# Kernel optimization log

Hardware: AMD Instinct MI355X
Metric: run time of the kernel (lower is better)

Reference implementation:

```python
import jax, jax.numpy as jnp
import numpy as np
from jax import lax

# ---- static config (mirrors init_kwargs) ----
B, C, IMG, P = 8, 3, 512, 16
DIM, HEADS, DEPTH = 256, 8, 4
DH = DIM // HEADS            # 32 per-head dim
G = IMG // P                 # 32 patch grid
L = G * G                    # 1024 tokens
EC = DIM // 4                # 64 conv-embed channels
PD = (P // 4) ** 2 * EC      # 1024 = patch_dim


def layernorm(x, g, b):
    m = x.mean(-1, keepdims=True)
    v = x.var(-1, keepdims=True)
    return (x - m) / jnp.sqrt(v + 1e-5) * g + b


def setup_inputs() -> dict:
    key = jax.random.key(0)
    ks = jax.random.split(key, 10)
    return {
        "img": jax.random.normal(ks[0], (B, C, IMG, IMG), jnp.float32),
        "adj": jax.random.uniform(ks[1], (1, 1, L, L), jnp.float32),
        "label": jax.random.randint(ks[2], (B,), 0, 2),
        # ConvEmbed: Conv2d(3, 64, k=3, s=2, p=1) + BN + GELU + MaxPool(3, s=2, p=1)
        "conv_w": jax.random.normal(ks[3], (EC, C, 3, 3), jnp.float32) * 0.1,
        "conv_b": jnp.zeros((EC,), jnp.float32),
        "bn_g": jnp.ones((EC,), jnp.float32),
        "bn_b": jnp.zeros((EC,), jnp.float32),
        # patch_to_embedding: Linear(PD, DIM)
        "emb_w": jax.random.normal(ks[4], (PD, DIM), jnp.float32) * 0.02,
        "emb_b": jnp.zeros((DIM,), jnp.float32),
        # per-layer params (leading DEPTH axis)
        "ln_g": jnp.ones((DEPTH, DIM), jnp.float32),
        "ln_b": jnp.zeros((DEPTH, DIM), jnp.float32),
        "qk_w": jax.random.normal(ks[5], (DEPTH, DH, 2 * DH), jnp.float32) * 0.1,
        "qk_b": jnp.zeros((DEPTH, 2 * DH), jnp.float32),
        "v_w": jax.random.normal(ks[6], (DEPTH, DH, DH), jnp.float32) * 0.1,
        "v_b": jnp.zeros((DEPTH, DH), jnp.float32),
        "proj_w": jax.random.normal(ks[7], (DEPTH, DIM, DIM), jnp.float32) * 0.05,
    }


def _forward(img, adj, conv_w, conv_b, bn_g, bn_b, emb_w, emb_b,
             ln_g, ln_b, qk_w, qk_b, v_w, v_b, proj_w):
    b = img.shape[0]
    # 'b c (h p1) (w p2) -> (b h w) c p1 p2'
    x = img.reshape(b, C, G, P, G, P).transpose(0, 2, 4, 1, 3, 5).reshape(b * L, C, P, P)
    # ConvEmbed: conv(k3,s2,p1) -> BN(train stats) -> GELU -> maxpool(k3,s2,p1)
    x = lax.conv_general_dilated(x, conv_w, (2, 2), ((1, 1), (1, 1)),
                                 dimension_numbers=("NCHW", "OIHW", "NCHW"))
    x = x + conv_b[None, :, None, None]
    mu = x.mean((0, 2, 3), keepdims=True)
    var = x.var((0, 2, 3), keepdims=True)
    x = (x - mu) / jnp.sqrt(var + 1e-5) * bn_g[None, :, None, None] + bn_b[None, :, None, None]
    x = jax.nn.gelu(x, approximate=False)
    x = lax.reduce_window(x, -jnp.inf, lax.max, (1, 1, 3, 3), (1, 1, 2, 2),
                          ((0, 0), (0, 0), (1, 1), (1, 1)))
    # '(b s) c p1 p2 -> b s (c p1 p2)' then Linear(PD, DIM)
    x = x.reshape(b, L, PD)
    x = x @ emb_w + emb_b                       # (b, L, DIM)
    A = adj[0, 0]                               # (L, L), shared across batch & heads
    scale = DIM ** -0.5
    attn = None
    for i in range(DEPTH):
        xn = layernorm(x, ln_g[i], ln_b[i])     # PreNorm
        xh = xn.reshape(b, L, HEADS, DH).transpose(0, 2, 1, 3)  # b h t d
        # GIN qk: MLP((A @ x) + x) -> 2*DH per head, chunk into q, k
        m = jnp.einsum("st,bhtd->bhsd", A, xh) + xh
        qk = jax.nn.relu(m @ qk_w[i] + qk_b[i])  # (b,h,L,2*DH)
        q, k = qk[..., :DH], qk[..., DH:]
        score = jnp.einsum("bhld,bhtd->bhlt", q, k) * scale
        attn = jax.nn.softmax(score / 2, axis=-1)  # norm_attn_score (b,h,L,L)
        # GIN v driven by the attention matrix as adjacency
        mv = jnp.einsum("bhst,bhtd->bhsd", attn, xh) + xh
        v = jax.nn.relu(mv @ v_w[i] + v_b[i])      # (b,h,L,DH)
        v = jax.nn.gelu(v.transpose(0, 2, 1, 3).reshape(b, L, DIM), approximate=False)
        x = v @ proj_w[i] + xn                     # Residual adds the NORMED input
    return attn


def reference(img, adj, label, conv_w, conv_b, bn_g, bn_b, emb_w, emb_b,
              ln_g, ln_b, qk_w, qk_b, v_w, v_b, proj_w):
    # label is unused in the original forward
    return _forward(img, adj, conv_w, conv_b, bn_g, bn_b, emb_w, emb_b,
                    ln_g, ln_b, qk_w, qk_b, v_w, v_b, proj_w)
```

## Files before the change

kernel.cpp:

```cpp
#include <hip/hip_runtime.h>
#include <hip/hip_bf16.h>
#include <math.h>

typedef __hip_bfloat16 bf16;
typedef __attribute__((ext_vector_type(8))) short bf16x8;
typedef __attribute__((ext_vector_type(4))) float f32x4;

#define MFMA(a,b,c) __builtin_amdgcn_mfma_f32_16x16x32_bf16(a,b,c,0,0,0)

#define B_ 8
#define C_ 3
#define IMG_ 512
#define P_ 16
#define DIM_ 256
#define HEADS_ 8
#define DEPTH_ 4
#define DH_ 32
#define L_ 1024
#define EC_ 64
#define PD_ 1024
#define NPATCH 8192
#define NROWS 65536

__device__ __forceinline__ float ldsel(const void* p, long i, int m){
    return m ? __bfloat162float(((const bf16*)p)[i]) : ((const float*)p)[i];
}
__device__ __forceinline__ float geluf(float x){
    return 0.5f * x * (1.0f + erff(x * 0.70710678118654752f));
}
__device__ __forceinline__ short f2bf_s(float f){
    bf16 h = __float2bfloat16(f); return *(short*)&h;
}
__device__ __forceinline__ float bfs2f(short s){
    bf16 h = *(bf16*)&s; return __bfloat162float(h);
}
__device__ __forceinline__ void split2(float f, short& hi, short& lo){
    hi = f2bf_s(f);
    lo = f2bf_s(f - bfs2f(hi));
}
__device__ __forceinline__ void split3(float f, short& h, short& m, short& l){
    h = f2bf_s(f); float r1 = f - bfs2f(h);
    m = f2bf_s(r1); float r2 = r1 - bfs2f(m);
    l = f2bf_s(r2);
}

__global__ void detect_kernel(const void* __restrict__ img, int* __restrict__ flag)
{
    const unsigned* w = (const unsigned*)img;
    const int t = threadIdx.x;
    int c = 0;
    #pragma unroll
    for (int i = 0; i < 4; i++){
        unsigned b = (w[t*4 + i] >> 7) & 0xFFu;
        if (b >= 100u && b <= 145u) c++;
    }
    #pragma unroll
    for (int o = 32; o > 0; o >>= 1) c += __shfl_xor(c, o, 64);
    if (t == 0) *flag = (c > 180) ? 1 : 0;
}

__global__ void conv_stats_kernel(const int* __restrict__ fl,
                                  const void* __restrict__ img,
                                  const void* __restrict__ conv_w,
                                  const void* __restrict__ conv_b,
                                  float* __restrict__ psum, float* __restrict__ psq)
{
    const int f = *fl;
    __shared__ float inp[3*18*18];
    __shared__ float wl[EC_*27];
    __shared__ float reds[4][64], redq[4][64];
    const int n = blockIdx.x, t = threadIdx.x;
    const int b = n >> 10, l = n & 1023;
    const int gy = l >> 5, gx = l & 31;
    const int w = t >> 6, o = t & 63;
    for (int e = t; e < EC_*27; e += 256) wl[e] = ldsel(conv_w, e, f);
    for (int e = t; e < 3*18*18; e += 256){
        int c = e / 324, rem = e - c*324;
        int y = rem / 18, x = rem - y*18;
        float v = 0.f;
        if (y >= 1 && y <= 16 && x >= 1 && x <= 16)
            v = ldsel(img, ((long)(b*C_+c)*IMG_ + gy*P_ + (y-1))*IMG_ + gx*P_ + (x-1), f);
        inp[e] = v;
    }
    __syncthreads();
    float wr[27];
    #pragma unroll
    for (int i = 0; i < 27; i++) wr[i] = wl[o*27 + i];
    const float cb = ldsel(conv_b, o, f);
    float s = 0.f, sq = 0.f;
    #pragma unroll
    for (int i = 0; i < 16; i++){
        int pix = w*16 + i;
        int oy = pix >> 3, ox = pix & 7;
        float acc = cb;
        #pragma unroll
        for (int c = 0; c < 3; c++)
        #pragma unroll
        for (int ky = 0; ky < 3; ky++)
        #pragma unroll
        for (int kx = 0; kx < 3; kx++)
            acc += inp[c*324 + (2*oy+ky)*18 + 2*ox+kx] * wr[c*9+ky*3+kx];
        s += acc; sq += acc*acc;
    }
    reds[w][o] = s; redq[w][o] = sq;
    __syncthreads();
    if (t < 64){
        float S = reds[0][t]+reds[1][t]+reds[2][t]+reds[3][t];
        float Q = redq[0][t]+redq[1][t]+redq[2][t]+redq[3][t];
        psum[(long)t*NPATCH + n] = S;
        psq [(long)t*NPATCH + n] = Q;
    }
}

__global__ void bn_stats_kernel(const int* __restrict__ fl,
                                const float* __restrict__ psum, const float* __restrict__ psq,
                                const void* __restrict__ bn_g, const void* __restrict__ bn_b,
                                float* __restrict__ scaleA, float* __restrict__ biasA)
{
    const int f = *fl;
    __shared__ float rs[256], rq[256];
    const int o = blockIdx.x, t = threadIdx.x;
    float S = 0.f, Q = 0.f;
    for (int n = t; n < NPATCH; n += 256){ S += psum[(long)o*NPATCH+n]; Q += psq[(long)o*NPATCH+n]; }
    rs[t] = S; rq[t] = Q; __syncthreads();
    for (int st = 128; st > 0; st >>= 1){
        if (t < st){ rs[t] += rs[t+st]; rq[t] += rq[t+st]; }
        __syncthreads();
    }
    if (t == 0){
        const float Ninv = 1.0f / (float)((long)NPATCH * 64);
        float mean = rs[0] * Ninv;
        float var  = rq[0] * Ninv - mean*mean;
        float rstd = rsqrtf(var + 1e-5f);
        float sc = ldsel(bn_g, o, f) * rstd;
        scaleA[o] = sc;
        biasA[o]  = ldsel(bn_b, o, f) - mean*sc;
    }
}

__global__ void bn_gelu_pool_kernel(const int* __restrict__ fl,
                                    const void* __restrict__ img,
                                    const void* __restrict__ conv_w,
                                    const void* __restrict__ conv_b,
                                    const float* __restrict__ scaleA,
                                    const float* __restrict__ biasA,
                                    short* __restrict__ x0h, short* __restrict__ x0m,
                                    short* __restrict__ x0l)
{
    const int f = *fl;
    __shared__ float inp[3*18*18];
    __shared__ float wl[EC_*27];
    __shared__ float cosb[64][65];
    __shared__ float poolb[64*17];
    __shared__ float sA[64], bA[64];
    const int n = blockIdx.x, t = threadIdx.x;
    const int b = n >> 10, l = n & 1023;
    const int gy = l >> 5, gx = l & 31;
    const int w = t >> 6, o = t & 63;
    for (int e = t; e < EC_*27; e += 256) wl[e] = ldsel(conv_w, e, f);
    for (int e = t; e < 3*18*18; e += 256){
        int c = e / 324, rem = e - c*324;
        int y = rem / 18, x = rem - y*18;
        float v = 0.f;
        if (y >= 1 && y <= 16 && x >= 1 && x <= 16)
            v = ldsel(img, ((long)(b*C_+c)*IMG_ + gy*P_ + (y-1))*IMG_ + gx*P_ + (x-1), f);
        inp[e] = v;
    }
    if (t < 64){ sA[t] = scaleA[t]; bA[t] = biasA[t]; }
    __syncthreads();
    float wr[27];
    #pragma unroll
    for (int i = 0; i < 27; i++) wr[i] = wl[o*27 + i];
    const float cb = ldsel(conv_b, o, f);
    const float sc = sA[o], bb = bA[o];
    #pragma unroll
    for (int i = 0; i < 16; i++){
        int pix = w*16 + i;
        int oy = pix >> 3, ox = pix & 7;
        float acc = cb;
        #pragma unroll
        for (int c = 0; c < 3; c++)
        #pragma unroll
        for (int ky = 0; ky < 3; ky++)
        #pragma unroll
        for (int kx = 0; kx < 3; kx++)
            acc += inp[c*324 + (2*oy+ky)*18 + 2*ox+kx] * wr[c*9+ky*3+kx];
        cosb[pix][o] = geluf(acc*sc + bb);
    }
    __syncthreads();
    #pragma unroll
    for (int j = 0; j < 4; j++){
        int pp = w*4 + j;
        int py = pp >> 2, px = pp & 3;
        int y0 = max(0, 2*py-1), y1 = min(7, 2*py+1);
        int xs = max(0, 2*px-1), x1 = min(7, 2*px+1);
        float mx = -INFINITY;
        for (int y = y0; y <= y1; y++)
            for (int x = xs; x <= x1; x++)
                mx = fmaxf(mx, cosb[y*8+x][o]);
        poolb[o*17 + pp] = mx;
    }
    __syncthreads();
    for (int e = t; e < 1024; e += 256){
        float v = poolb[(e>>4)*17 + (e&15)];
        short h, m, lo; split3(v, h, m, lo);
        long idx = (long)n*PD_ + e;
        x0h[idx] = h; x0m[idx] = m; x0l[idx] = lo;
    }
}

__global__ void split_adj_kernel(const int* __restrict__ fl, const void* __restrict__ adj,
                                 short* __restrict__ Ah, short* __restrict__ Am,
                                 short* __restrict__ Al)
{
    const int f = *fl;
    long i = (long)blockIdx.x*256 + threadIdx.x;
    short h, m, l; split3(ldsel(adj, i, f), h, m, l);
    Ah[i] = h; Am[i] = m; Al[i] = l;
}

__global__ void tsplit_kernel(const int* __restrict__ fl, const void* __restrict__ src,
                              long soff, int R, int Ccols,
                              short* __restrict__ oh, short* __restrict__ om,
                              short* __restrict__ ol)
{
    __shared__ float tile[64][65];
    const int f = *fl;
    const int t = threadIdx.x;
    const int c0 = blockIdx.x*64, r0 = blockIdx.y*64;
    for (int e = t; e < 4096; e += 256){
        int r = e >> 6, c = e & 63;
        tile[r][c] = ldsel(src, soff + (long)(r0+r)*Ccols + c0+c, f);
    }
    __syncthreads();
    const int ch = t >> 2, lg = t & 3;
    long ob = (long)(c0+ch)*R + r0 + lg*16;
    bf16x8 h0,h1,m0,m1,l0,l1;
    #pragma unroll
    for (int i = 0; i < 8; i++){
        short h,m,l;
        split3(tile[lg*16+i][ch], h,m,l);    h0[i]=h; m0[i]=m; l0[i]=l;
        split3(tile[lg*16+8+i][ch], h,m,l);  h1[i]=h; m1[i]=m; l1[i]=l;
    }
    *(bf16x8*)(oh+ob) = h0; *(bf16x8*)(oh+ob+8) = h1;
    *(bf16x8*)(om+ob) = m0; *(bf16x8*)(om+ob+8) = m1;
    *(bf16x8*)(ol+ob) = l0; *(bf16x8*)(ol+ob+8) = l1;
}

__global__ void ln_repack_kernel(const int* __restrict__ fl,
                                 const float* __restrict__ x,
                                 const void* __restrict__ g, long goff,
                                 const void* __restrict__ beta, long boff,
                                 float* __restrict__ xn,
                                 short* __restrict__ xTh, short* __restrict__ xTm,
                                 short* __restrict__ xTl)
{
    __shared__ float tile[32][257];
    __shared__ float gs[256], bs[256];
    __shared__ float pm[8][32], pq[8][32];
    __shared__ float mean_s[32], rstd_s[32];
    const int f = *fl;
    const int t = threadIdx.x;
    const int r0 = blockIdx.x*32;
    const int b = r0 >> 10, l0 = r0 & 1023;
    gs[t] = ldsel(g, goff + t, f);
    bs[t] = ldsel(beta, boff + t, f);
    for (int e = t; e < 32*256; e += 256){
        int r = e >> 8, c = e & 255;
        tile[r][c] = x[(long)(r0+r)*DIM_ + c];
    }
    __syncthreads();
    {
        int row = t & 31, part = t >> 5;
        float s = 0.f, q = 0.f;
        #pragma unroll
        for (int c = 0; c < 32; c++){
            float v = tile[row][part*32 + c];
            s += v; q += v*v;
        }
        pm[part][row] = s; pq[part][row] = q;
    }
    __syncthreads();
    if (t < 32){
        float S = 0.f, Q = 0.f;
        #pragma unroll
        for (int p2 = 0; p2 < 8; p2++){ S += pm[p2][t]; Q += pq[p2][t]; }
        float mean = S * (1.0f/256.0f);
        float var  = Q * (1.0f/256.0f) - mean*mean;
        mean_s[t] = mean;
        rstd_s[t] = rsqrtf(var + 1e-5f);
    }
    __syncthreads();
    for (int e = t; e < 32*256; e += 256){
        int r = e >> 8, c = e & 255;
        float v = (tile[r][c] - mean_s[r])*rstd_s[r]*gs[c] + bs[c];
        tile[r][c] = v;
        xn[(long)(r0+r)*DIM_ + c] = v;
    }
    __syncthreads();
    const int half = t & 1, cB = t >> 1;
    #pragma unroll
    for (int gp = 0; gp < 2; gp++){
        int c = gp*128 + cB;
        long ob = ((long)(b*DIM_) + c)*L_ + l0 + half*16;
        bf16x8 h0, m0, l0v;
        #pragma unroll
        for (int i = 0; i < 8; i++){
            short hh, mm, ll;
            split3(tile[half*16 + i][c], hh, mm, ll);
            h0[i]=hh; m0[i]=mm; l0v[i]=ll;
        }
        *(bf16x8*)(xTh+ob) = h0; *(bf16x8*)(xTm+ob) = m0; *(bf16x8*)(xTl+ob) = l0v;
        bf16x8 h1, m1, l1v;
        #pragma unroll
        for (int i = 0; i < 8; i++){
            short hh, mm, ll;
            split3(tile[half*16 + 8 + i][c], hh, mm, ll);
            h1[i]=hh; m1[i]=mm; l1v[i]=ll;
        }
        *(bf16x8*)(xTh+ob+8) = h1; *(bf16x8*)(xTm+ob+8) = m1; *(bf16x8*)(xTl+ob+8) = l1v;
    }
}

__global__ __launch_bounds__(256)
void mfma_gemm(const short* __restrict__ Ah, const short* __restrict__ Am,
               const short* __restrict__ Al, long strAb,
               const short* __restrict__ Bh, const short* __restrict__ Bm,
               const short* __restrict__ Bl, long strBb,
               const void* __restrict__ bias, long biasOff, const int* __restrict__ fl,
               const float* __restrict__ Dadd, long strDb,
               float* __restrict__ C, long strCb,
               int N, int K)
{
    const int t = threadIdx.x;
    const int w = t >> 6, lane = t & 63;
    const int mrow = lane & 15, quad = lane >> 4;
    const int wr = w & 1, wc = w >> 1;
    const int s0 = blockIdx.y*32 + wr*16;
    const int n0 = blockIdx.x*128 + wc*64;
    const int z = blockIdx.z;
    const short* Ahp = Ah + (long)z*strAb;
    const short* Amp = Am + (long)z*strAb;
    const short* Alp = Al + (long)z*strAb;
    const short* Bhp = Bh + (long)z*strBb;
    const short* Bmp = Bm + (long)z*strBb;
    const short* Blp = Bl + (long)z*strBb;
    f32x4 acc[4];
    #pragma unroll
    for (int i = 0; i < 4; i++) acc[i] = (f32x4){0.f,0.f,0.f,0.f};

    const long aoff0 = (long)(s0 + mrow)*K + quad*8;
    const long b0    = (long)(n0 + mrow)*K + quad*8;
    const long bstp  = (long)16*K;

    bf16x8 ahA, amA, alA, bhA[4], bmA[4], blA[4];
    ahA = *(const bf16x8*)(Ahp + aoff0);
    amA = *(const bf16x8*)(Amp + aoff0);
    alA = *(const bf16x8*)(Alp + aoff0);
    #pragma unroll
    for (int nt = 0; nt < 4; nt++){
        long bo = b0 + nt*bstp;
        bhA[nt] = *(const bf16x8*)(Bhp + bo);
        bmA[nt] = *(const bf16x8*)(Bmp + bo);
        blA[nt] = *(const bf16x8*)(Blp + bo);
    }
    for (int k0 = 0; k0 < K; k0 += 64){
        bf16x8 ahB, amB, alB, bhB[4], bmB[4], blB[4];
        {
            long an = aoff0 + k0 + 32;
            ahB = *(const bf16x8*)(Ahp + an);
            amB = *(const bf16x8*)(Amp + an);
            alB = *(const bf16x8*)(Alp + an);
            #pragma unroll
            for (int nt = 0; nt < 4; nt++){
                long bo = b0 + nt*bstp + k0 + 32;
                bhB[nt] = *(const bf16x8*)(Bhp + bo);
                bmB[nt] = *(const bf16x8*)(Bmp + bo);
                blB[nt] = *(const bf16x8*)(Blp + bo);
            }
        }
        #pragma unroll
        for (int nt = 0; nt < 4; nt++){
            acc[nt] = MFMA(alA, bhA[nt], acc[nt]);
            acc[nt] = MFMA(amA, bmA[nt], acc[nt]);
            acc[nt] = MFMA(ahA, blA[nt], acc[nt]);
            acc[nt] = MFMA(amA, bhA[nt], acc[nt]);
            acc[nt] = MFMA(ahA, bmA[nt], acc[nt]);
            acc[nt] = MFMA(ahA, bhA[nt], acc[nt]);
        }
        if (k0 + 64 < K){
            long an = aoff0 + k0 + 64;
            ahA = *(const bf16x8*)(Ahp + an);
            amA = *(const bf16x8*)(Amp + an);
            alA = *(const bf16x8*)(Alp + an);
            #pragma unroll
            for (int nt = 0; nt < 4; nt++){
                long bo = b0 + nt*bstp + k0 + 64;
                bhA[nt] = *(const bf16x8*)(Bhp + bo);
                bmA[nt] = *(const bf16x8*)(Bmp + bo);
                blA[nt] = *(const bf16x8*)(Blp + bo);
            }
        }
        #pragma unroll
        for (int nt = 0; nt < 4; nt++){
            acc[nt] = MFMA(alB, bhB[nt], acc[nt]);
            acc[nt] = MFMA(amB, bmB[nt], acc[nt]);
            acc[nt] = MFMA(ahB, blB[nt], acc[nt]);
            acc[nt] = MFMA(amB, bhB[nt], acc[nt]);
            acc[nt] = MFMA(ahB, bmB[nt], acc[nt]);
            acc[nt] = MFMA(ahB, bhB[nt], acc[nt]);
        }
    }
    const int f = *fl;
    #pragma unroll
    for (int nt = 0; nt < 4; nt++)
    #pragma unroll
    for (int r = 0; r < 4; r++){
        long row = s0 + quad*4 + r;
        int col = n0 + nt*16 + mrow;
        float v = acc[nt][r];
        if (bias) v += ldsel(bias, biasOff + col, f);
        if (Dadd) v += Dadd[(long)z*strDb + row*N + col];
        C[(long)z*strCb + row*N + col] = v;
    }
}

__global__ __launch_bounds__(256)
void gemm_axn_qk(const short* __restrict__ Ah, const short* __restrict__ Am,
                 const short* __restrict__ Al,
                 const short* __restrict__ Bh, const short* __restrict__ Bm,
                 const short* __restrict__ Bl,
                 const float* __restrict__ xn, const int* __restrict__ fl,
                 const void* __restrict__ qk_w, long woff,
                 const void* __restrict__ qk_b, long boff,
                 short* __restrict__ qh, short* __restrict__ qm, short* __restrict__ ql,
                 short* __restrict__ kh, short* __restrict__ km, short* __restrict__ kl,
                 short* __restrict__ q2h, short* __restrict__ q2m,
                 short* __restrict__ k2h, short* __restrict__ k2m)
{
    __shared__ float m_lds[32][132];
    __shared__ float wl[32][65];
    __shared__ float bl2[64];
    const int t = threadIdx.x;
    const int w = t >> 6, lane = t & 63;
    const int mrow = lane & 15, quad = lane >> 4;
    const int wr = w & 1, wc = w >> 1;
    const int s0 = blockIdx.y*32 + wr*16;
    const int n0 = blockIdx.x*128;
    const int nc = n0 + wc*64;
    const int z = blockIdx.z;
    const int f = *fl;
    for (int e = t; e < 2048; e += 256) wl[e>>6][e&63] = ldsel(qk_w, woff + e, f);
    if (t < 64) bl2[t] = ldsel(qk_b, boff + t, f);

    const short* Bhp = Bh + (long)z*DIM_*L_;
    const short* Bmp = Bm + (long)z*DIM_*L_;
    const short* Blp = Bl + (long)z*DIM_*L_;
    f32x4 acc[4];
    #pragma unroll
    for (int i = 0; i < 4; i++) acc[i] = (f32x4){0.f,0.f,0.f,0.f};

    const long aoff0 = (long)(s0 + mrow)*L_ + quad*8;
    const long b0    = (long)(nc + mrow)*L_ + quad*8;
    const long bstp  = (long)16*L_;

    bf16x8 ahA, amA, alA, bhA[4], bmA[4], blA[4];
    ahA = *(const bf16x8*)(Ah + aoff0);
    amA = *(const bf16x8*)(Am + aoff0);
    alA = *(const bf16x8*)(Al + aoff0);
    #pragma unroll
    for (int nt = 0; nt < 4; nt++){
        long bo = b0 + nt*bstp;
        bhA[nt] = *(const bf16x8*)(Bhp + bo);
        bmA[nt] = *(const bf16x8*)(Bmp + bo);
        blA[nt] = *(const bf16x8*)(Blp + bo);
    }
    for (int k0 = 0; k0 < L_; k0 += 64){
        bf16x8 ahB, amB, alB, bhB[4], bmB[4], blB[4];
        {
            long an = aoff0 + k0 + 32;
            ahB = *(const bf16x8*)(Ah + an);
            amB = *(const bf16x8*)(Am + an);
            alB = *(const bf16x8*)(Al + an);
            #pragma unroll
            for (int nt = 0; nt < 4; nt++){
                long bo = b0 + nt*bstp + k0 + 32;
                bhB[nt] = *(const bf16x8*)(Bhp + bo);
                bmB[nt] = *(const bf16x8*)(Bmp + bo);
                blB[nt] = *(const bf16x8*)(Blp + bo);
            }
        }
        #pragma unroll
        for (int nt = 0; nt < 4; nt++){
            acc[nt] = MFMA(alA, bhA[nt], acc[nt]);
            acc[nt] = MFMA(amA, bmA[nt], acc[nt]);
            acc[nt] = MFMA(ahA, blA[nt], acc[nt]);
            acc[nt] = MFMA(amA, bhA[nt], acc[nt]);
            acc[nt] = MFMA(ahA, bmA[nt], acc[nt]);
            acc[nt] = MFMA(ahA, bhA[nt], acc[nt]);
        }
        if (k0 + 64 < L_){
            long an = aoff0 + k0 + 64;
            ahA = *(const bf16x8*)(Ah + an);
            amA = *(const bf16x8*)(Am + an);
            alA = *(const bf16x8*)(Al + an);
            #pragma unroll
            for (int nt = 0; nt < 4; nt++){
                long bo = b0 + nt*bstp + k0 + 64;
                bhA[nt] = *(const bf16x8*)(Bhp + bo);
                bmA[nt] = *(const bf16x8*)(Bmp + bo);
                blA[nt] = *(const bf16x8*)(Blp + bo);
            }
        }
        #pragma unroll
        for (int nt = 0; nt < 4; nt++){
            acc[nt] = MFMA(alB, bhB[nt], acc[nt]);
            acc[nt] = MFMA(amB, bmB[nt], acc[nt]);
            acc[nt] = MFMA(ahB, blB[nt], acc[nt]);
            acc[nt] = MFMA(amB, bhB[nt], acc[nt]);
            acc[nt] = MFMA(ahB, bmB[nt], acc[nt]);
            acc[nt] = MFMA(ahB, bhB[nt], acc[nt]);
        }
    }
    #pragma unroll
    for (int nt = 0; nt < 4; nt++)
    #pragma unroll
    for (int r = 0; r < 4; r++){
        long row = s0 + quad*4 + r;
        int col = nc + nt*16 + mrow;
        m_lds[wr*16 + quad*4 + r][wc*64 + nt*16 + mrow] =
            acc[nt][r] + xn[((long)(z*L_) + row)*DIM_ + col];
    }
    __syncthreads();
    const int j = lane;
    float wreg[32];
    #pragma unroll
    for (int d = 0; d < 32; d++) wreg[d] = wl[d][j];
    const float bj = bl2[j];
    const int hgl = (n0 >> 5) + w;
    #pragma unroll
    for (int rr = 0; rr < 32; rr++){
        const float* mp = &m_lds[rr][w*32];
        float a = bj;
        #pragma unroll
        for (int d = 0; d < 32; d += 4){
            f32x4 m4 = *(const f32x4*)(mp + d);
            a += m4[0]*wreg[d] + m4[1]*wreg[d+1] + m4[2]*wreg[d+2] + m4[3]*wreg[d+3];
        }
        a = fmaxf(a, 0.f);
        long rg = ((long)(z*HEADS_ + hgl))*L_ + blockIdx.y*32 + rr;
        if (q2h){
            short hh2, mm2; split2(a, hh2, mm2);
            if (j < 32){ q2h[rg*DH_+j]=hh2; q2m[rg*DH_+j]=mm2; }
            else { int d2 = j-32; k2h[rg*DH_+d2]=hh2; k2m[rg*DH_+d2]=mm2; }
        } else {
            short hh2, mm2, ll2; split3(a, hh2, mm2, ll2);
            if (j < 32){ qh[rg*DH_+j]=hh2; qm[rg*DH_+j]=mm2; ql[rg*DH_+j]=ll2; }
            else { int d2 = j-32; kh[rg*DH_+d2]=hh2; km[rg*DH_+d2]=mm2; kl[rg*DH_+d2]=ll2; }
        }
    }
}

__global__ __launch_bounds__(256)
void attn_mfma_kernel(const short* __restrict__ qh3, const short* __restrict__ qm3,
                      const short* __restrict__ ql3,
                      const short* __restrict__ kh3, const short* __restrict__ km3,
                      const short* __restrict__ kl3,
                      const short* __restrict__ q2h, const short* __restrict__ q2m,
                      const short* __restrict__ k2h, const short* __restrict__ k2m,
                      const short* __restrict__ xTh, const short* __restrict__ xTm,
                      const float* __restrict__ xn, const int* __restrict__ fl,
                      const void* __restrict__ v_w, long vwoff,
                      const void* __restrict__ v_b, long vboff,
                      short* __restrict__ v2h, short* __restrict__ v2m,
                      short* __restrict__ v2l,
                      float* __restrict__ attn_out)
{
    __shared__ float pt[4][16][37];
    __shared__ float mv_lds[64][36];
    __shared__ float wv[32][33];
    __shared__ float vb[32];
    const int t = threadIdx.x;
    const int w = t >> 6, lane = t & 63;
    const int mrow = lane & 15, quad = lane >> 4;
    const int bh = blockIdx.y, b = bh >> 3, h = bh & 7;
    const int s0 = blockIdx.x*64 + w*16;
    const bool last = (attn_out != nullptr);
    const float inv32 = 1.0f/32.0f;
    const long kb = (long)bh*L_*DH_;

    if (!last){
        const int f = *fl;
        for (int e = t; e < 1024; e += 256) wv[e>>5][e&31] = ldsel(v_w, vwoff + e, f);
        if (t < 32) vb[t] = ldsel(v_b, vboff + t, f);
    }

    bf16x8 a_h, a_m, a_l;
    {
        long qoff = ((long)bh*L_ + s0 + mrow)*DH_ + quad*8;
        if (last){
            a_h = *(const bf16x8*)(q2h + qoff);
            a_m = *(const bf16x8*)(q2m + qoff);
        } else {
            a_h = *(const bf16x8*)(qh3 + qoff);
            a_m = *(const bf16x8*)(qm3 + qoff);
            a_l = *(const bf16x8*)(ql3 + qoff);
        }
    }

    float m_run[4] = {-INFINITY,-INFINITY,-INFINITY,-INFINITY};
    float lsum[4] = {0.f,0.f,0.f,0.f};
    f32x4 pv[2];
    pv[0] = (f32x4){0.f,0.f,0.f,0.f};
    pv[1] = (f32x4){0.f,0.f,0.f,0.f};

    bf16x8 kAh[2], kAm[2], kAl[2];
    #pragma unroll
    for (int u = 0; u < 2; u++){
        long koff = kb + (long)(u*16 + mrow)*DH_ + quad*8;
        if (last){
            kAh[u] = *(const bf16x8*)(k2h + koff);
            kAm[u] = *(const bf16x8*)(k2m + koff);
        } else {
            kAh[u] = *(const bf16x8*)(kh3 + koff);
            kAm[u] = *(const bf16x8*)(km3 + koff);
            kAl[u] = *(const bf16x8*)(kl3 + koff);
        }
    }

    for (int pr = 0; pr < 32; pr++){
        bf16x8 kBh[2], kBm[2], kBl[2];
        if (pr < 31){
            #pragma unroll
            for (int u = 0; u < 2; u++){
                long koff = kb + (long)(((pr+1)*2+u)*16 + mrow)*DH_ + quad*8;
                if (last){
                    kBh[u] = *(const bf16x8*)(k2h + koff);
                    kBm[u] = *(const bf16x8*)(k2m + koff);
                } else {
                    kBh[u] = *(const bf16x8*)(kh3 + koff);
                    kBm[u] = *(const bf16x8*)(km3 + koff);
                    kBl[u] = *(const bf16x8*)(kl3 + koff);
                }
            }
        }
        bf16x8 xh8[2], xl8[2];
        if (!last){
            int j0 = pr*32;
            #pragma unroll
            for (int nt = 0; nt < 2; nt++){
                long xoff = ((long)(b*DIM_) + h*DH_ + nt*16 + mrow)*L_ + j0 + quad*8;
                xh8[nt] = *(const bf16x8*)(xTh + xoff);
                xl8[nt] = *(const bf16x8*)(xTm + xoff);
            }
        }
        f32x4 acc[2];
        #pragma unroll
        for (int u = 0; u < 2; u++){
            f32x4 a1 = (f32x4){0.f,0.f,0.f,0.f};
            f32x4 a2 = (f32x4){0.f,0.f,0.f,0.f};
            if (last){
                a1 = MFMA(a_m, kAh[u], a1);
                a1 = MFMA(a_h, kAm[u], a1);
                a2 = MFMA(a_h, kAh[u], a2);
            } else {
                a1 = MFMA(a_l, kAh[u], a1);
                a1 = MFMA(a_m, kAm[u], a1);
                a1 = MFMA(a_h, kAl[u], a1);
                a2 = MFMA(a_m, kAh[u], a2);
                a2 = MFMA(a_h, kAm[u], a2);
                a2 = MFMA(a_h, kAh[u], a2);
            }
            acc[u] = a1 + a2;
        }
        float tmv[4];
        #pragma unroll
        for (int r = 0; r < 4; r++){
            float tm = fmaxf(acc[0][r], acc[1][r]);
            tm = fmaxf(tm, __shfl_xor(tm, 1, 64));
            tm = fmaxf(tm, __shfl_xor(tm, 2, 64));
            tm = fmaxf(tm, __shfl_xor(tm, 4, 64));
            tm = fmaxf(tm, __shfl_xor(tm, 8, 64));
            tmv[r] = tm;
        }
        bool need = (tmv[0] > m_run[0] + 32.f) | (tmv[1] > m_run[1] + 32.f)
                  | (tmv[2] > m_run[2] + 32.f) | (tmv[3] > m_run[3] + 32.f);
        if (__ballot(need)){
            #pragma unroll
            for (int r = 0; r < 4; r++){
                float mnew = fmaxf(m_run[r], tmv[r]);
                float sc = __expf((m_run[r] - mnew) * inv32);
                lsum[r] *= sc; pv[0][r] *= sc; pv[1][r] *= sc;
                m_run[r] = mnew;
            }
        }
        #pragma unroll
        for (int r = 0; r < 4; r++){
            float p0 = __expf((acc[0][r] - m_run[r]) * inv32);
            float p1 = __expf((acc[1][r] - m_run[r]) * inv32);
            lsum[r] += p0 + p1;
            if (!last){
                pt[w][quad*4 + r][mrow]      = p0;
                pt[w][quad*4 + r][16 + mrow] = p1;
            }
        }
        if (!last){
            const float* pp = &pt[w][mrow][quad*8];
            bf16x8 phi, plo;
            #pragma unroll
            for (int jj = 0; jj < 8; jj++){
                short hh, ll; split2(pp[jj], hh, ll);
                phi[jj] = hh; plo[jj] = ll;
            }
            #pragma unroll
            for (int nt = 0; nt < 2; nt++){
                pv[nt] = MFMA(plo, xh8[nt], pv[nt]);
                pv[nt] = MFMA(phi, xl8[nt], pv[nt]);
                pv[nt] = MFMA(phi, xh8[nt], pv[nt]);
            }
        }
        if (pr < 31){
            #pragma unroll
            for (int u = 0; u < 2; u++){
                kAh[u] = kBh[u]; kAm[u] = kBm[u];
                if (!last) kAl[u] = kBl[u];
            }
        }
    }
    #pragma unroll
    for (int r = 0; r < 4; r++){
        lsum[r] += __shfl_xor(lsum[r], 1, 64);
        lsum[r] += __shfl_xor(lsum[r], 2, 64);
        lsum[r] += __shfl_xor(lsum[r], 4, 64);
        lsum[r] += __shfl_xor(lsum[r], 8, 64);
    }
    float linv[4];
    #pragma unroll
    for (int r = 0; r < 4; r++) linv[r] = 1.0f / lsum[r];

    if (!last){
        #pragma unroll
        for (int nt = 0; nt < 2; nt++)
        #pragma unroll
        for (int r = 0; r < 4; r++){
            int lrow = w*16 + quad*4 + r;
            long row = s0 + quad*4 + r;
            float resid = xn[((long)(b*L_) + row)*DIM_ + h*DH_ + nt*16 + mrow];
            mv_lds[lrow][nt*16 + mrow] = pv[nt][r]*linv[r] + resid;
        }
        __syncthreads();
        const int j = lane & 31, rh = lane >> 5;
        float wreg[32];
        #pragma unroll
        for (int d = 0; d < 32; d++) wreg[d] = wv[d][j];
        const float vbj = vb[j];
        #pragma unroll
        for (int rr = 0; rr < 8; rr++){
            int lrow = w*16 + rh*8 + rr;
            const float* mp = &mv_lds[lrow][0];
            float a = vbj;
            #pragma unroll
            for (int d = 0; d < 32; d += 4){
                f32x4 m4 = *(const f32x4*)(mp + d);
                a += m4[0]*wreg[d] + m4[1]*wreg[d+1] + m4[2]*wreg[d+2] + m4[3]*wreg[d+3];
            }
            a = geluf(fmaxf(a, 0.f));
            int l = blockIdx.x*64 + lrow;
            long idx = ((long)(b*L_) + l)*DIM_ + h*DH_ + j;
            short hh2, mm2, ll2; split3(a, hh2, mm2, ll2);
            v2h[idx] = hh2; v2m[idx] = mm2; v2l[idx] = ll2;
        }
    } else {
        long koff0 = kb + (long)mrow*DH_ + quad*8;
        bf16x8 pAh = *(const bf16x8*)(k2h + koff0);
        bf16x8 pAm = *(const bf16x8*)(k2m + koff0);
        for (int ct = 0; ct < 64; ct++){
            bf16x8 pBh, pBm;
            if (ct < 63){
                long koff = kb + (long)((ct+1)*16 + mrow)*DH_ + quad*8;
                pBh = *(const bf16x8*)(k2h + koff);
                pBm = *(const bf16x8*)(k2m + koff);
            }
            f32x4 a1 = (f32x4){0.f,0.f,0.f,0.f};
            f32x4 a2 = (f32x4){0.f,0.f,0.f,0.f};
            a1 = MFMA(a_m, pAh, a1);
            a1 = MFMA(a_h, pAm, a1);
            a2 = MFMA(a_h, pAh, a2);
            f32x4 a = a1 + a2;
            #pragma unroll
            for (int r = 0; r < 4; r++){
                float pn = __expf((a[r] - m_run[r]) * inv32) * linv[r];
                attn_out[((long)bh*L_ + s0 + quad*4 + r)*L_ + ct*16 + mrow] = pn;
            }
            if (ct < 63){ pAh = pBh; pAm = pBm; }
        }
    }
}

extern "C" void kernel_launch(void* const* d_in, const int* in_sizes, int n_in,
                              void* d_out, int out_size, void* d_ws, size_t ws_size,
                              hipStream_t stream)
{
    const int o = (n_in >= 16) ? 3 : 2;
    const void* img    = d_in[0];
    const void* adj    = d_in[1];
    const void* conv_w = d_in[o+0];
    const void* conv_b = d_in[o+1];
    const void* bn_g   = d_in[o+2];
    const void* bn_b   = d_in[o+3];
    const void* emb_w  = d_in[o+4];
    const void* emb_b  = d_in[o+5];
    const void* ln_g   = d_in[o+6];
    const void* ln_b   = d_in[o+7];
    const void* qk_w   = d_in[o+8];
    const void* qk_b   = d_in[o+9];
    const void* v_w    = d_in[o+10];
    const void* v_b    = d_in[o+11];
    const void* proj_w = d_in[o+12];
    float* attn_out = (float*)d_out;

    float* S = (float*)d_out;
    const long M1 = 1L << 20;
    float* x     = S;
    float* xn    = S + 2*M1;
    short* sp    = (short*)(S + 6*M1);
    short* adjh  = sp;
    short* adjm  = sp + 1*M1;
    short* adjl  = sp + 2*M1;
    short* embTh = sp + 3*M1;
    short* embTm = embTh + 262144;
    short* embTl = embTm + 262144;
    short* lp    = (short*)(S + 8*M1);
    short* xTh   = lp;
    short* xTm   = lp + 2*M1;
    short* xTl   = lp + 4*M1;
    short* qh3   = lp + 6*M1;
    short* qm3   = lp + 8*M1;
    short* ql3   = lp + 10*M1;
    short* kh3   = lp + 12*M1;
    short* km3   = lp + 14*M1;
    short* kl3   = lp + 16*M1;
    short* v2h   = lp + 18*M1;
    short* v2m   = lp + 20*M1;
    short* v2l   = lp + 22*M1;
    short* pTh   = lp + 24*M1;
    short* pTm   = pTh + 65536;
    short* pTl   = pTm + 65536;
    float* psum  = S + 24*M1;
    float* psq   = psum + (long)EC_*NPATCH;
    short* x0h   = (short*)(S + 41*M1);
    short* x0m   = x0h + 8*M1;
    short* x0l   = x0m + 8*M1;

    float* wsf   = (float*)d_ws;
    int*   flag  = (int*)wsf;
    float* scaleA= wsf + 64;
    float* biasA = wsf + 128;
    short* q2h   = (short*)(wsf + 256);
    short* q2m   = q2h + 2*M1;
    short* k2h   = q2m + 2*M1;
    short* k2m   = k2h + 2*M1;

    detect_kernel<<<1, 64, 0, stream>>>(img, flag);
    split_adj_kernel<<<L_*L_/256, 256, 0, stream>>>(flag, adj, adjh, adjm, adjl);
    tsplit_kernel<<<dim3(4,16), 256, 0, stream>>>(flag, emb_w, 0, PD_, DIM_, embTh, embTm, embTl);
    conv_stats_kernel<<<NPATCH, 256, 0, stream>>>(flag, img, conv_w, conv_b, psum, psq);
    bn_stats_kernel<<<EC_, 256, 0, stream>>>(flag, psum, psq, bn_g, bn_b, scaleA, biasA);
    bn_gelu_pool_kernel<<<NPATCH, 256, 0, stream>>>(flag, img, conv_w, conv_b,
                                                    scaleA, biasA, x0h, x0m, x0l);

    mfma_gemm<<<dim3(2,256,1), 256, 0, stream>>>(
        x0h, x0m, x0l, 0,  embTh, embTm, embTl, 0,
        emb_b, 0, flag,  nullptr, 0,  x, 0,  DIM_, PD_);

    for (int i = 0; i < DEPTH_; i++){
        const bool last = (i == DEPTH_-1);
        ln_repack_kernel<<<NROWS/32/8, 256, 0, stream>>>(flag, x,
            ln_g, (long)i*DIM_, ln_b, (long)i*DIM_, xn, xTh, xTm, xTl);
        gemm_axn_qk<<<dim3(2,32,8), 256, 0, stream>>>(
            adjh, adjm, adjl,  xTh, xTm, xTl,  xn, flag,
            qk_w, (long)i*DH_*2*DH_, qk_b, (long)i*2*DH_,
            qh3, qm3, ql3, kh3, km3, kl3,
            last ? q2h : nullptr, last ? q2m : nullptr,
            last ? k2h : nullptr, last ? k2m : nullptr);
        attn_mfma_kernel<<<dim3(16, B_*HEADS_), 256, 0, stream>>>(
            qh3, qm3, ql3, kh3, km3, kl3, q2h, q2m, k2h, k2m,
            xTh, xTm, xn, flag,
            v_w, (long)i*DH_*DH_, v_b, (long)i*DH_,
            v2h, v2m, v2l,
            last ? attn_out : nullptr);
        if (!last){
            tsplit_kernel<<<dim3(4,4), 256, 0, stream>>>(flag, proj_w,
                (long)i*DIM_*DIM_, DIM_, DIM_, pTh, pTm, pTl);
            mfma_gemm<<<dim3(2,256,1), 256, 0, stream>>>(
                v2h, v2m, v2l, 0,  pTh, pTm, pTl, 0,
                nullptr, 0, flag,  xn, 0,  x, 0,  DIM_, DIM_);
        }
    }
}
```

Measured before the change: 1.765 ms.

## Halve GEMM N-tile to double grid size and hoist proj_w splits

The MFMA GEMM and the adjacency-times-x/qk GEMM now use 64-column tiles per block instead of 128, doubling the number of blocks and halving per-wave accumulators and B-operand registers. The goal is better CU occupancy and wave parallelism on the 256-wide GEMMs. In exchange, each A-tile load is reused by fewer MFMAs, which raises redundant A traffic. The qk epilogue is reworked so each wave processes half the rows for one head. Separately, the three per-layer proj_w transpose-splits are merged into one batched launch before the layer loop, removing three launches from the critical path.

Measured after the change: 1.828 ms. 3.6% more time.

```diff
diff --git a/kernel.cpp b/kernel.cpp
--- a/kernel.cpp
+++ b/kernel.cpp
@@ -220,17 +220,20 @@
 }
 
 __global__ void tsplit_kernel(const int* __restrict__ fl, const void* __restrict__ src,
-                              long soff, int R, int Ccols,
+                              long soff, long zsStride, int R, int Ccols,
                               short* __restrict__ oh, short* __restrict__ om,
-                              short* __restrict__ ol)
+                              short* __restrict__ ol, long ozStride)
 {
     __shared__ float tile[64][65];
     const int f = *fl;
     const int t = threadIdx.x;
+    const int zz = blockIdx.z;
+    const long sb = soff + (long)zz*zsStride;
+    oh += (long)zz*ozStride; om += (long)zz*ozStride; ol += (long)zz*ozStride;
     const int c0 = blockIdx.x*64, r0 = blockIdx.y*64;
     for (int e = t; e < 4096; e += 256){
         int r = e >> 6, c = e & 63;
-        tile[r][c] = ldsel(src, soff + (long)(r0+r)*Ccols + c0+c, f);
+        tile[r][c] = ldsel(src, sb + (long)(r0+r)*Ccols + c0+c, f);
     }
     __syncthreads();
     const int ch = t >> 2, lg = t & 3;
@@ -337,7 +340,7 @@
     const int mrow = lane & 15, quad = lane >> 4;
     const int wr = w & 1, wc = w >> 1;
     const int s0 = blockIdx.y*32 + wr*16;
-    const int n0 = blockIdx.x*128 + wc*64;
+    const int n0 = blockIdx.x*64 + wc*32;
     const int z = blockIdx.z;
     const short* Ahp = Ah + (long)z*strAb;
     const short* Amp = Am + (long)z*strAb;
@@ -345,34 +348,34 @@
     const short* Bhp = Bh + (long)z*strBb;
     const short* Bmp = Bm + (long)z*strBb;
     const short* Blp = Bl + (long)z*strBb;
-    f32x4 acc[4];
-    #pragma unroll
-    for (int i = 0; i < 4; i++) acc[i] = (f32x4){0.f,0.f,0.f,0.f};
+    f32x4 acc[2];
+    acc[0] = (f32x4){0.f,0.f,0.f,0.f};
+    acc[1] = (f32x4){0.f,0.f,0.f,0.f};
 
     const long aoff0 = (long)(s0 + mrow)*K + quad*8;
     const long b0    = (long)(n0 + mrow)*K + quad*8;
     const long bstp  = (long)16*K;
 
-    bf16x8 ahA, amA, alA, bhA[4], bmA[4], blA[4];
+    bf16x8 ahA, amA, alA, bhA[2], bmA[2], blA[2];
     ahA = *(const bf16x8*)(Ahp + aoff0);
     amA = *(const bf16x8*)(Amp + aoff0);
     alA = *(const bf16x8*)(Alp + aoff0);
     #pragma unroll
-    for (int nt = 0; nt < 4; nt++){
+    for (int nt = 0; nt < 2; nt++){
         long bo = b0 + nt*bstp;
         bhA[nt] = *(const bf16x8*)(Bhp + bo);
         bmA[nt] = *(const bf16x8*)(Bmp + bo);
         blA[nt] = *(const bf16x8*)(Blp + bo);
     }
     for (int k0 = 0; k0 < K; k0 += 64){
-        bf16x8 ahB, amB, alB, bhB[4], bmB[4], blB[4];
+        bf16x8 ahB, amB, alB, bhB[2], bmB[2], blB[2];
         {
             long an = aoff0 + k0 + 32;
             ahB = *(const bf16x8*)(Ahp + an);
             amB = *(const bf16x8*)(Amp + an);
             alB = *(const bf16x8*)(Alp + an);
             #pragma unroll
-            for (int nt = 0; nt < 4; nt++){
+            for (int nt = 0; nt < 2; nt++){
                 long bo = b0 + nt*bstp + k0 + 32;
                 bhB[nt] = *(const bf16x8*)(Bhp + bo);
                 bmB[nt] = *(const bf16x8*)(Bmp + bo);
@@ -380,7 +383,7 @@
             }
         }
         #pragma unroll
-        for (int nt = 0; nt < 4; nt++){
+        for (int nt = 0; nt < 2; nt++){
             acc[nt] = MFMA(alA, bhA[nt], acc[nt]);
             acc[nt] = MFMA(amA, bmA[nt], acc[nt]);
             acc[nt] = MFMA(ahA, blA[nt], acc[nt]);
@@ -394,7 +397,7 @@
             amA = *(const bf16x8*)(Amp + an);
             alA = *(const bf16x8*)(Alp + an);
             #pragma unroll
-            for (int nt = 0; nt < 4; nt++){
+            for (int nt = 0; nt < 2; nt++){
                 long bo = b0 + nt*bstp + k0 + 64;
                 bhA[nt] = *(const bf16x8*)(Bhp + bo);
                 bmA[nt] = *(const bf16x8*)(Bmp + bo);
@@ -402,7 +405,7 @@
             }
         }
         #pragma unroll
-        for (int nt = 0; nt < 4; nt++){
+        for (int nt = 0; nt < 2; nt++){
             acc[nt] = MFMA(alB, bhB[nt], acc[nt]);
             acc[nt] = MFMA(amB, bmB[nt], acc[nt]);
             acc[nt] = MFMA(ahB, blB[nt], acc[nt]);
@@ -413,7 +416,7 @@
     }
     const int f = *fl;
     #pragma unroll
-    for (int nt = 0; nt < 4; nt++)
+    for (int nt = 0; nt < 2; nt++)
     #pragma unroll
     for (int r = 0; r < 4; r++){
         long row = s0 + quad*4 + r;
@@ -438,7 +441,7 @@
                  short* __restrict__ q2h, short* __restrict__ q2m,
                  short* __restrict__ k2h, short* __restrict__ k2m)
 {
-    __shared__ float m_lds[32][132];
+    __shared__ float m_lds[32][68];
     __shared__ float wl[32][65];
     __shared__ float bl2[64];
     const int t = threadIdx.x;
@@ -446,8 +449,8 @@
     const int mrow = lane & 15, quad = lane >> 4;
     const int wr = w & 1, wc = w >> 1;
     const int s0 = blockIdx.y*32 + wr*16;
-    const int n0 = blockIdx.x*128;
-    const int nc = n0 + wc*64;
+    const int n0 = blockIdx.x*64;
+    const int nc = n0 + wc*32;
     const int z = blockIdx.z;
     const int f = *fl;
     for (int e = t; e < 2048; e += 256) wl[e>>6][e&63] = ldsel(qk_w, woff + e, f);
@@ -456,34 +459,34 @@
     const short* Bhp = Bh + (long)z*DIM_*L_;
     const short* Bmp = Bm + (long)z*DIM_*L_;
     const short* Blp = Bl + (long)z*DIM_*L_;
-    f32x4 acc[4];
-    #pragma unroll
-    for (int i = 0; i < 4; i++) acc[i] = (f32x4){0.f,0.f,0.f,0.f};
+    f32x4 acc[2];
+    acc[0] = (f32x4){0.f,0.f,0.f,0.f};
+    acc[1] = (f32x4){0.f,0.f,0.f,0.f};
 
     const long aoff0 = (long)(s0 + mrow)*L_ + quad*8;
     const long b0    = (long)(nc + mrow)*L_ + quad*8;
     const long bstp  = (long)16*L_;
 
-    bf16x8 ahA, amA, alA, bhA[4], bmA[4], blA[4];
+    bf16x8 ahA, amA, alA, bhA[2], bmA[2], blA[2];
     ahA = *(const bf16x8*)(Ah + aoff0);
     amA = *(const bf16x8*)(Am + aoff0);
     alA = *(const bf16x8*)(Al + aoff0);
     #pragma unroll
-    for (int nt = 0; nt < 4; nt++){
+    for (int nt = 0; nt < 2; nt++){
         long bo = b0 + nt*bstp;
         bhA[nt] = *(const bf16x8*)(Bhp + bo);
         bmA[nt] = *(const bf16x8*)(Bmp + bo);
         blA[nt] = *(const bf16x8*)(Blp + bo);
     }
     for (int k0 = 0; k0 < L_; k0 += 64){
-        bf16x8 ahB, amB, alB, bhB[4], bmB[4], blB[4];
+        bf16x8 ahB, amB, alB, bhB[2], bmB[2], blB[2];
         {
             long an = aoff0 + k0 + 32;
             ahB = *(const bf16x8*)(Ah + an);
             amB = *(const bf16x8*)(Am + an);
             alB = *(const bf16x8*)(Al + an);
             #pragma unroll
-            for (int nt = 0; nt < 4; nt++){
+            for (int nt = 0; nt < 2; nt++){
                 long bo = b0 + nt*bstp + k0 + 32;
                 bhB[nt] = *(const bf16x8*)(Bhp + bo);
                 bmB[nt] = *(const bf16x8*)(Bmp + bo);
@@ -491,7 +494,7 @@
             }
         }
         #pragma unroll
-        for (int nt = 0; nt < 4; nt++){
+        for (int nt = 0; nt < 2; nt++){
             acc[nt] = MFMA(alA, bhA[nt], acc[nt]);
             acc[nt] = MFMA(amA, bmA[nt], acc[nt]);
             acc[nt] = MFMA(ahA, blA[nt], acc[nt]);
@@ -505,7 +508,7 @@
             amA = *(const bf16x8*)(Am + an);
             alA = *(const bf16x8*)(Al + an);
             #pragma unroll
-            for (int nt = 0; nt < 4; nt++){
+            for (int nt = 0; nt < 2; nt++){
                 long bo = b0 + nt*bstp + k0 + 64;
                 bhA[nt] = *(const bf16x8*)(Bhp + bo);
                 bmA[nt] = *(const bf16x8*)(Bmp + bo);
@@ -513,7 +516,7 @@
             }
         }
         #pragma unroll
-        for (int nt = 0; nt < 4; nt++){
+        for (int nt = 0; nt < 2; nt++){
             acc[nt] = MFMA(alB, bhB[nt], acc[nt]);
             acc[nt] = MFMA(amB, bmB[nt], acc[nt]);
             acc[nt] = MFMA(ahB, blB[nt], acc[nt]);
@@ -523,12 +526,12 @@
         }
     }
     #pragma unroll
-    for (int nt = 0; nt < 4; nt++)
+    for (int nt = 0; nt < 2; nt++)
     #pragma unroll
     for (int r = 0; r < 4; r++){
         long row = s0 + quad*4 + r;
         int col = nc + nt*16 + mrow;
-        m_lds[wr*16 + quad*4 + r][wc*64 + nt*16 + mrow] =
+        m_lds[wr*16 + quad*4 + r][wc*32 + nt*16 + mrow] =
             acc[nt][r] + xn[((long)(z*L_) + row)*DIM_ + col];
     }
     __syncthreads();
@@ -537,10 +540,12 @@
     #pragma unroll
     for (int d = 0; d < 32; d++) wreg[d] = wl[d][j];
     const float bj = bl2[j];
-    const int hgl = (n0 >> 5) + w;
-    #pragma unroll
-    for (int rr = 0; rr < 32; rr++){
-        const float* mp = &m_lds[rr][w*32];
+    const int hl = w & 1, rh = w >> 1;
+    const int hgl = (n0 >> 5) + hl;
+    #pragma unroll
+    for (int rr = 0; rr < 16; rr++){
+        const int lrow = rh*16 + rr;
+        const float* mp = &m_lds[lrow][hl*32];
         float a = bj;
         #pragma unroll
         for (int d = 0; d < 32; d += 4){
@@ -548,7 +553,7 @@
             a += m4[0]*wreg[d] + m4[1]*wreg[d+1] + m4[2]*wreg[d+2] + m4[3]*wreg[d+3];
         }
         a = fmaxf(a, 0.f);
-        long rg = ((long)(z*HEADS_ + hgl))*L_ + blockIdx.y*32 + rr;
+        long rg = ((long)(z*HEADS_ + hgl))*L_ + blockIdx.y*32 + lrow;
         if (q2h){
             short hh2, mm2; split2(a, hh2, mm2);
             if (j < 32){ q2h[rg*DH_+j]=hh2; q2m[rg*DH_+j]=mm2; }
@@ -844,8 +849,8 @@
     short* v2m   = lp + 20*M1;
     short* v2l   = lp + 22*M1;
     short* pTh   = lp + 24*M1;
-    short* pTm   = pTh + 65536;
-    short* pTl   = pTm + 65536;
+    short* pTm   = pTh + 3*65536;
+    short* pTl   = pTm + 3*65536;
     float* psum  = S + 24*M1;
     float* psq   = psum + (long)EC_*NPATCH;
     short* x0h   = (short*)(S + 41*M1);
@@ -863,13 +868,16 @@
 
     detect_kernel<<<1, 64, 0, stream>>>(img, flag);
     split_adj_kernel<<<L_*L_/256, 256, 0, stream>>>(flag, adj, adjh, adjm, adjl);
-    tsplit_kernel<<<dim3(4,16), 256, 0, stream>>>(flag, emb_w, 0, PD_, DIM_, embTh, embTm, embTl);
+    tsplit_kernel<<<dim3(4,16,1), 256, 0, stream>>>(flag, emb_w, 0, 0, PD_, DIM_,
+                                                    embTh, embTm, embTl, 0);
+    tsplit_kernel<<<dim3(4,4,3), 256, 0, stream>>>(flag, proj_w, 0, (long)DIM_*DIM_,
+                                                   DIM_, DIM_, pTh, pTm, pTl, 65536);
     conv_stats_kernel<<<NPATCH, 256, 0, stream>>>(flag, img, conv_w, conv_b, psum, psq);
     bn_stats_kernel<<<EC_, 256, 0, stream>>>(flag, psum, psq, bn_g, bn_b, scaleA, biasA);
     bn_gelu_pool_kernel<<<NPATCH, 256, 0, stream>>>(flag, img, conv_w, conv_b,
                                                     scaleA, biasA, x0h, x0m, x0l);
 
-    mfma_gemm<<<dim3(2,256,1), 256, 0, stream>>>(
+    mfma_gemm<<<dim3(4,256,1), 256, 0, stream>>>(
         x0h, x0m, x0l, 0,  embTh, embTm, embTl, 0,
         emb_b, 0, flag,  nullptr, 0,  x, 0,  DIM_, PD_);
 
@@ -877,7 +885,7 @@
         const bool last = (i == DEPTH_-1);
         ln_repack_kernel<<<NROWS/32/8, 256, 0, stream>>>(flag, x,
             ln_g, (long)i*DIM_, ln_b, (long)i*DIM_, xn, xTh, xTm, xTl);
-        gemm_axn_qk<<<dim3(2,32,8), 256, 0, stream>>>(
+        gemm_axn_qk<<<dim3(4,32,8), 256, 0, stream>>>(
             adjh, adjm, adjl,  xTh, xTm, xTl,  xn, flag,
             qk_w, (long)i*DH_*2*DH_, qk_b, (long)i*2*DH_,
             qh3, qm3, ql3, kh3, km3, kl3,
@@ -890,10 +898,9 @@
             v2h, v2m, v2l,
             last ? attn_out : nullptr);
         if (!last){
-            tsplit_kernel<<<dim3(4,4), 256, 0, stream>>>(flag, proj_w,
-                (long)i*DIM_*DIM_, DIM_, DIM_, pTh, pTm, pTl);
-            mfma_gemm<<<dim3(2,256,1), 256, 0, stream>>>(
-                v2h, v2m, v2l, 0,  pTh, pTm, pTl, 0,
+            mfma_gemm<<<dim3(4,256,1), 256, 0, stream>>>(
+                v2h, v2m, v2l, 0,
+                pTh + (long)i*65536, pTm + (long)i*65536, pTl + (long)i*65536, 0,
                 nullptr, 0, flag,  xn, 0,  x, 0,  DIM_, DIM_);
         }
     }
```
